# Kernel tuning notes

Measured on AMD Instinct MI355X. Metric: run time of the kernel, lower is better.

## Reference

```python
import jax, jax.numpy as jnp
import numpy as np

V, E, HT, HC = 30000, 300, 256, 256
B, LC, T = 32, 32, 64
NTAG = 9  # output_dim + 2


def lstm_dir(x, lens, Wih, Whh, b, reverse):
    """Variable-length single-direction LSTM (packed-sequence semantics).
    x: [N, T, D], lens: [N] int. Returns outputs [N, T, H] zeroed at pad steps.
    Masked state update keeps h,c frozen at pad steps, so reverse=True starts
    from each sequence's true last element (zeros carry through leading pads).
    """
    N, Tn, _ = x.shape
    H = Whh.shape[1]
    gx = jnp.einsum('ntd,gd->ntg', x, Wih) + b            # [N,T,4H]
    mask = jnp.arange(Tn)[None, :] < lens[:, None]         # [N,T]

    def step(carry, inp):
        h, c = carry
        g_t, m = inp                                       # [N,4H], [N]
        gates = g_t + h @ Whh.T
        i, f, g, o = jnp.split(gates, 4, axis=-1)
        c_new = jax.nn.sigmoid(f) * c + jax.nn.sigmoid(i) * jnp.tanh(g)
        h_new = jax.nn.sigmoid(o) * jnp.tanh(c_new)
        m = m[:, None]
        h2 = jnp.where(m, h_new, h)
        c2 = jnp.where(m, c_new, c)
        return (h2, c2), jnp.where(m, h2, 0.0)

    init = (jnp.zeros((N, H), x.dtype), jnp.zeros((N, H), x.dtype))
    xs = (jnp.swapaxes(gx, 0, 1), mask.T)
    _, ys = jax.lax.scan(step, init, xs, reverse=reverse)
    return jnp.swapaxes(ys, 0, 1)                          # [N,T,H]


def bilstm(x, lens, Wih_f, Whh_f, b_f, Wih_b, Whh_b, b_b):
    hf = lstm_dir(x, lens, Wih_f, Whh_f, b_f, reverse=False)
    hb = lstm_dir(x, lens, Wih_b, Whh_b, b_b, reverse=True)
    return jnp.concatenate([hf, hb], axis=-1)


def setup_inputs() -> dict:
    key = jax.random.key(0)
    ks = jax.random.split(key, 20)
    s = 0.05
    inp = {
        'x': jax.random.randint(ks[0], (B, LC, T), 0, V, dtype=jnp.int32),
        'x_feats': jax.random.normal(ks[1], (B, LC, 64), jnp.float32),
        'x_len': jnp.maximum(jax.random.randint(ks[2], (B,), 0, LC, dtype=jnp.int32), 1),
        'x_chunk_len': jax.random.randint(ks[3], (B, LC), 1, T + 1, dtype=jnp.int32),
        'emb': jax.random.normal(ks[4], (V, E), jnp.float32) * s,
        'tok_Wih_f': jax.random.normal(ks[5], (4 * HT, E), jnp.float32) * s,
        'tok_Whh_f': jax.random.normal(ks[6], (4 * HT, HT), jnp.float32) * s,
        'tok_b_f': jax.random.normal(ks[7], (4 * HT,), jnp.float32) * s,
        'tok_Wih_b': jax.random.normal(ks[8], (4 * HT, E), jnp.float32) * s,
        'tok_Whh_b': jax.random.normal(ks[9], (4 * HT, HT), jnp.float32) * s,
        'tok_b_b': jax.random.normal(ks[10], (4 * HT,), jnp.float32) * s,
        'chk_Wih_f': jax.random.normal(ks[11], (4 * HC, 2 * HT), jnp.float32) * s,
        'chk_Whh_f': jax.random.normal(ks[12], (4 * HC, HC), jnp.float32) * s,
        'chk_b_f': jax.random.normal(ks[13], (4 * HC,), jnp.float32) * s,
        'chk_Wih_b': jax.random.normal(ks[14], (4 * HC, 2 * HT), jnp.float32) * s,
        'chk_Whh_b': jax.random.normal(ks[15], (4 * HC, HC), jnp.float32) * s,
        'chk_b_b': jax.random.normal(ks[16], (4 * HC,), jnp.float32) * s,
        'fc_W': jax.random.normal(ks[17], (NTAG, 2 * HC), jnp.float32) * s,
        'fc_b': jax.random.normal(ks[18], (NTAG,), jnp.float32) * s,
    }
    return inp


def reference(x, x_feats, x_len, x_chunk_len, emb,
              tok_Wih_f, tok_Whh_f, tok_b_f, tok_Wih_b, tok_Whh_b, tok_b_b,
              chk_Wih_f, chk_Whh_f, chk_b_f, chk_Wih_b, chk_Whh_b, chk_b_b,
              fc_W, fc_b):
    b, lc, t = x.shape
    xe = emb[x].reshape(b * lc, t, -1)                     # [B*LC, T, E]
    clens = jnp.clip(x_chunk_len.reshape(-1), 1, t)        # [B*LC]
    h = bilstm(xe, clens, tok_Wih_f, tok_Whh_f, tok_b_f,
               tok_Wih_b, tok_Whh_b, tok_b_b)              # [B*LC, T, 2HT]
    # gather output at last valid timestep (= [fwd final, bwd one-step])
    last = h[jnp.arange(b * lc), clens - 1]                # [B*LC, 2HT]
    chunks = last.reshape(b, lc, -1)                       # [B, LC, 2HT]
    ch = bilstm(chunks, x_len, chk_Wih_f, chk_Whh_f, chk_b_f,
                chk_Wih_b, chk_Whh_b, chk_b_b)             # [B, LC, 2HC]
    # pad_packed(total_length=LC) gives zeros at pad -> fc sees zeros there
    out = ch @ fc_W.T + fc_b                               # [B, LC, NTAG]
    return out
```

## Files before the change

kernel.cpp:

```cpp
#include <hip/hip_runtime.h>


typedef __attribute__((ext_vector_type(8))) short s16x8;
typedef __attribute__((ext_vector_type(4))) float f32x4;
typedef __attribute__((ext_vector_type(2))) unsigned int u32x2;

__device__ __forceinline__ unsigned short f2bf(float f) {
  unsigned u = __builtin_bit_cast(unsigned, f);
  u += 0x7fff + ((u >> 16) & 1);
  return (unsigned short)(u >> 16);
}
__device__ __forceinline__ float bf2f(unsigned short h) {
  unsigned u = ((unsigned)h) << 16;
  return __builtin_bit_cast(float, u);
}
__device__ __forceinline__ float sigm(float x) { return 1.f / (1.f + __expf(-x)); }
__device__ __forceinline__ float tanh_(float x) { return 1.f - 2.f / (__expf(2.f * x) + 1.f); }

union PK8 { s16x8 v; unsigned short u[8]; };

__global__ void prep_weights(const float* __restrict__ wihf, const float* __restrict__ wihb,
                             const float* __restrict__ wcf, const float* __restrict__ wcb,
                             unsigned short* __restrict__ o_wf, unsigned short* __restrict__ o_wb,
                             unsigned short* __restrict__ o_wcf, unsigned short* __restrict__ o_wcb) {
  const int job = blockIdx.y, r = blockIdx.x, tid = threadIdx.x;
  const float* src; unsigned short* dst; int Ks, Kd;
  switch (job) {
    case 0: src = wihf; dst = o_wf;   Ks = 300; Kd = 320; break;
    case 1: src = wihb; dst = o_wb;   Ks = 300; Kd = 320; break;
    case 2: src = wcf;  dst = o_wcf;  Ks = 512; Kd = 512; break;
    default:src = wcb;  dst = o_wcb;  Ks = 512; Kd = 512; break;
  }
  for (int c = tid; c < Kd; c += 256)
    dst[r * Kd + c] = f2bf(c < Ks ? src[r * Ks + c] : 0.f);
}

__global__ __launch_bounds__(256)
void prep_whh_frag(const float* __restrict__ w0, const float* __restrict__ w1,
                   const float* __restrict__ w2,
                   unsigned short* __restrict__ o0, unsigned short* __restrict__ o1,
                   unsigned short* __restrict__ o2) {
  const float* src = blockIdx.y == 0 ? w0 : (blockIdx.y == 1 ? w1 : w2);
  unsigned short* dst = blockIdx.y == 0 ? o0 : (blockIdx.y == 1 ? o1 : o2);
  const int fid = blockIdx.x;
  const int b = fid & 1, g = (fid >> 1) & 3, kt = (fid >> 3) & 7, js = fid >> 6;
  for (int i = threadIdx.x; i < 512; i += 256) {
    const int lane = i >> 3, e = i & 7;
    const int cc = lane & 15, qq = lane >> 4;
    const int row = g * 256 + (js * 2 + b) * 16 + cc;
    const int col = kt * 32 + qq * 8 + e;
    dst[(size_t)fid * 512 + i] = f2bf(src[row * 256 + col]);
  }
}

__global__ void prep_small(const int* __restrict__ x, const int* __restrict__ xcl,
                           int* __restrict__ clens, int* __restrict__ lastv,
                           int* __restrict__ order, int* __restrict__ glen) {
  __shared__ int start[65];
  const int n = threadIdx.x;
  if (n < 65) start[n] = 0;
  __syncthreads();
  int len = xcl[n]; len = len < 1 ? 1 : (len > 64 ? 64 : len);
  clens[n] = len;
  lastv[n] = x[n * 64 + len - 1];
  atomicAdd(&start[len], 1);
  __syncthreads();
  if (n == 0) {
    int acc = 0;
    for (int l = 64; l >= 1; --l) { int h = start[l]; start[l] = acc; acc += h; }
  }
  __syncthreads();
  int pos = atomicAdd(&start[len], 1);
  order[pos] = n;
  __syncthreads();
  if (n < 64) glen[n] = clens[order[n * 16]];
}

__global__ __launch_bounds__(256, 2)
void gemm_bf(const float* __restrict__ A, const int* __restrict__ rowmap,
             int Mrows, int Astride, int Klog, int KP,
             const unsigned short* __restrict__ B, unsigned short* __restrict__ C) {
  __shared__ unsigned short As[128 * 40];
// ... 64 lines not shown
    }
  }
  __syncthreads();
#pragma unroll
  for (int mt = 0; mt < 4; ++mt)
#pragma unroll
    for (int nt = 0; nt < 8; ++nt)
#pragma unroll
      for (int r = 0; r < 4; ++r)
        Ep[w][(mt * 16 + qq * 4 + r) * 136 + nt * 16 + cc] = f2bf(acc[mt][nt][r]);
  __syncthreads();
#pragma unroll
  for (int it = 0; it < 16; ++it) {
    int row = it * 4 + qq;
    s16x8 d = *(const s16x8*)&Ep[w][row * 136 + cc * 8];
    int gm = m0 + wrow * 64 + row;
    int gn = n0 + wcol * 128 + cc * 8;
    if (gm < Mrows) *(s16x8*)&C[(long)gm * 1024 + gn] = d;
  }
}

__global__ void bwd_step(const unsigned short* __restrict__ gxb,
                         const float* __restrict__ bias,
                         float* __restrict__ chunks) {
  const int n = blockIdx.x, j = threadIdx.x;
  const unsigned short* row = gxb + (long)n * 1024;
  float gi = bf2f(row[j]) + bias[j];
  float gg = bf2f(row[512 + j]) + bias[512 + j];
  float go = bf2f(row[768 + j]) + bias[768 + j];
  float cn = sigm(gi) * tanh_(gg);
  chunks[(long)n * 512 + 256 + j] = sigm(go) * tanh_(cn);
}

__global__ __launch_bounds__(256)
void gather_gx(const unsigned short* __restrict__ proj, const int* __restrict__ x,
               const int* __restrict__ order, const int* __restrict__ clens,
               const int* __restrict__ glen, const float* __restrict__ bias,
               unsigned short* __restrict__ gx) {
  const int t = blockIdx.x, p = blockIdx.y, j = threadIdx.x;
  if (t >= glen[p >> 4]) return;
  const int seq = order[p];
  const int len = clens[seq];
  if (t >= len) return;
  unsigned short* dst = gx + (((size_t)(p >> 4) * 64 + t) * 16 + (p & 15)) * 1024 + j * 4;
  const int tok = x[seq * 64 + t];
  const unsigned short* src = proj + (size_t)tok * 1024 + j;
  unsigned v0 = f2bf(bf2f(src[0]) + bias[j]);
  unsigned v1 = f2bf(bf2f(src[256]) + bias[256 + j]);
  unsigned v2 = f2bf(bf2f(src[512]) + bias[512 + j]);
  unsigned v3 = f2bf(bf2f(src[768]) + bias[768 + j]);
  u32x2 pk = {v0 | (v1 << 16), v2 | (v3 << 16)};
  *(u32x2*)dst = pk;
}

__global__ __launch_bounds__(256)
void repack4(const unsigned short* __restrict__ s0, const unsigned short* __restrict__ s1,
             const float* __restrict__ b0, const float* __restrict__ b1,
             unsigned short* __restrict__ d0, unsigned short* __restrict__ d1) {
  const int r = blockIdx.x, j = threadIdx.x;
  const int m = r >> 5, t = r & 31;
  const int mg = m >> 4, m16 = m & 15;
  const unsigned short* s = (blockIdx.y ? s1 : s0) + (size_t)r * 1024;
  const float* bb = blockIdx.y ? b1 : b0;
  unsigned short* d = (blockIdx.y ? d1 : d0) +
                      (size_t)((mg * 32 + t) * 16 + m16) * 1024 + j * 4;
  unsigned v0 = f2bf(bf2f(s[j]) + bb[j]);
  unsigned v1 = f2bf(bf2f(s[256 + j]) + bb[256 + j]);
  unsigned v2 = f2bf(bf2f(s[512 + j]) + bb[512 + j]);
  unsigned v3 = f2bf(bf2f(s[768 + j]) + bb[768 + j]);
  u32x2 pk = {v0 | (v1 << 16), v2 | (v3 << 16)};
  *(u32x2*)d = pk;
}

__global__ __launch_bounds__(1024, 4)
void tok_fwd(const unsigned short* __restrict__ gx,
             const unsigned short* __restrict__ WhP,
             const int* __restrict__ order,
             const int* __restrict__ clens,
             const int* __restrict__ glen,
             float* __restrict__ chunks) {
  extern __shared__ unsigned short smem[];
  unsigned short* hbuf = smem;
  unsigned short* ldsW = smem + 8448;
  int* sg = (int*)(smem + 8448 + 65536);
  int* slen = sg + 16;

  const int tid = threadIdx.x;
  const int lane = tid & 63, w = tid >> 6;
  const int cc = lane & 15, qq = lane >> 4;
  const int gb = blockIdx.x;

  if (tid < 16) {
    int s = order[gb * 16 + tid];
    sg[tid] = s;
    slen[tid] = clens[s];
  }
  for (int i = tid; i < 4224; i += 1024) hbuf[i] = 0;

  const unsigned short* wgl = WhP + ((size_t)(w >> 1) * 64 + (w & 1)) * 512 + lane * 8;
  {
    unsigned short* ld = ldsW + w * 4096 + lane * 8;
#pragma unroll
    for (int kt = 0; kt < 2; ++kt)
#pragma unroll
      for (int g = 0; g < 4; ++g)
        *(s16x8*)&ld[(kt * 4 + g) * 512] = *(const s16x8*)&wgl[(kt * 8 + g * 2) * 512];
  }
  s16x8 Rw[24];
#pragma unroll
  for (int kt = 2; kt < 8; ++kt)
#pragma unroll
    for (int g = 0; g < 4; ++g)
      Rw[(kt - 2) * 4 + g] = *(const s16x8*)&wgl[(kt * 8 + g * 2) * 512];

  __syncthreads();

  const int maxlen = glen[gb];
  const int j = w * 16 + cc;
  int lenr[4];
#pragma unroll
  for (int r = 0; r < 4; ++r) lenr[r] = slen[qq * 4 + r];

  float cst[4];
  unsigned short hreg[4];
#pragma unroll
  for (int r = 0; r < 4; ++r) { cst[r] = 0.f; hreg[r] = 0; }

  const unsigned short* gx0 = gx + (size_t)gb * 64 * 16 * 1024 + j * 4;
  const unsigned short* ldw = ldsW + w * 4096 + lane * 8;
  f32x4 zz = {0.f, 0.f, 0.f, 0.f};

  for (int t = 0; t < maxlen; ++t) {
    const unsigned short* hr = hbuf + (t & 1) * 4224;
    unsigned short* hw = hbuf + ((t & 1) ^ 1) * 4224;

    __syncthreads();

    u32x2 gxp[4];
#pragma unroll
    for (int r = 0; r < 4; ++r)
      gxp[r] = *(const u32x2*)(gx0 + ((size_t)t * 16 + qq * 4 + r) * 1024);

    f32x4 acc[4];
#pragma unroll
    for (int g = 0; g < 4; ++g) acc[g] = zz;

#pragma unroll
    for (int kt = 0; kt < 2; ++kt) {
      s16x8 a0 = *(const s16x8*)&hr[cc * 264 + kt * 32 + qq * 8];
#pragma unroll
      for (int g = 0; g < 4; ++g) {
        s16x8 bf = *(const s16x8*)&ldw[(kt * 4 + g) * 512];
        acc[g] = __builtin_amdgcn_mfma_f32_16x16x32_bf16(a0, bf, acc[g], 0, 0, 0);
      }
    }
#pragma unroll
    for (int kt = 2; kt < 8; ++kt) {
      s16x8 a0 = *(const s16x8*)&hr[cc * 264 + kt * 32 + qq * 8];
#pragma unroll
      for (int g = 0; g < 4; ++g)
        acc[g] = __builtin_amdgcn_mfma_f32_16x16x32_bf16(a0, Rw[(kt - 2) * 4 + g], acc[g], 0, 0, 0);
    }

#pragma unroll
    for (int r = 0; r < 4; ++r) {
      const int m = qq * 4 + r;
      const u32x2 pk = gxp[r];
      float gi = acc[0][r] + bf2f((unsigned short)(pk.x & 0xffff));
      float gf = acc[1][r] + bf2f((unsigned short)(pk.x >> 16));
      float gg = acc[2][r] + bf2f((unsigned short)(pk.y & 0xffff));
      float go = acc[3][r] + bf2f((unsigned short)(pk.y >> 16));
      if (t < lenr[r]) {
        float cn = sigm(gf) * cst[r] + sigm(gi) * tanh_(gg);
        cst[r] = cn;
        hreg[r] = f2bf(sigm(go) * tanh_(cn));
      }
      hw[m * 264 + j] = hreg[r];
    }
  }

#pragma unroll
  for (int r = 0; r < 4; ++r)
    chunks[(size_t)sg[qq * 4 + r] * 512 + j] = bf2f(hreg[r]);
}

__global__ __launch_bounds__(1024, 4)
void chunk_rec(const unsigned short* __restrict__ gxf,
               const unsigned short* __restrict__ gxb,
               const unsigned short* __restrict__ WhPf,
               const unsigned short* __restrict__ WhPb,
               const int* __restrict__ xlen,
               unsigned short* __restrict__ ch) {
  extern __shared__ unsigned short smem[];
  unsigned short* hbuf = smem;
  unsigned short* ldsW = smem + 8448;

  const int tid = threadIdx.x;
  const int lane = tid & 63, w = tid >> 6;
  const int cc = lane & 15, qq = lane >> 4;
  const int dir = blockIdx.x & 1, mg = blockIdx.x >> 1;
  const unsigned short* gx = (dir ? gxb : gxf) + (size_t)mg * 32 * 16 * 1024;
  const unsigned short* WhP = dir ? WhPb : WhPf;

  for (int i = tid; i < 4224; i += 1024) hbuf[i] = 0;

  const unsigned short* wgl = WhP + ((size_t)(w >> 1) * 64 + (w & 1)) * 512 + lane * 8;
  {
    unsigned short* ld = ldsW + w * 4096 + lane * 8;
#pragma unroll
    for (int kt = 0; kt < 2; ++kt)
#pragma unroll
      for (int g = 0; g < 4; ++g)
        *(s16x8*)&ld[(kt * 4 + g) * 512] = *(const s16x8*)&wgl[(kt * 8 + g * 2) * 512];
  }
  s16x8 Rw[24];
#pragma unroll
  for (int kt = 2; kt < 8; ++kt)
#pragma unroll
    for (int g = 0; g < 4; ++g)
      Rw[(kt - 2) * 4 + g] = *(const s16x8*)&wgl[(kt * 8 + g * 2) * 512];

  __syncthreads();

  const int j = w * 16 + cc;
  int lenr[4];
#pragma unroll
  for (int r = 0; r < 4; ++r) {
    int L = xlen[mg * 16 + qq * 4 + r];
    lenr[r] = L > 32 ? 32 : L;
  }

  float cst[4];
  unsigned short hreg[4];
#pragma unroll
  for (int r = 0; r < 4; ++r) { cst[r] = 0.f; hreg[r] = 0; }

  const unsigned short* ldw = ldsW + w * 4096 + lane * 8;
  f32x4 zz = {0.f, 0.f, 0.f, 0.f};

  for (int tt = 0; tt < 32; ++tt) {
    const int t = dir ? (31 - tt) : tt;
    const unsigned short* hr = hbuf + (tt & 1) * 4224;
    unsigned short* hw = hbuf + ((tt & 1) ^ 1) * 4224;

    __syncthreads();

    u32x2 gxp[4];
#pragma unroll
    for (int r = 0; r < 4; ++r)
      gxp[r] = *(const u32x2*)(gx + ((size_t)t * 16 + qq * 4 + r) * 1024 + j * 4);

    f32x4 acc[4];
#pragma unroll
    for (int g = 0; g < 4; ++g) acc[g] = zz;

#pragma unroll
    for (int kt = 0; kt < 2; ++kt) {
      s16x8 a0 = *(const s16x8*)&hr[cc * 264 + kt * 32 + qq * 8];
#pragma unroll
      for (int g = 0; g < 4; ++g) {
        s16x8 bf = *(const s16x8*)&ldw[(kt * 4 + g) * 512];
        acc[g] = __builtin_amdgcn_mfma_f32_16x16x32_bf16(a0, bf, acc[g], 0, 0, 0);
      }
    }
#pragma unroll
    for (int kt = 2; kt < 8; ++kt) {
      s16x8 a0 = *(const s16x8*)&hr[cc * 264 + kt * 32 + qq * 8];
#pragma unroll
      for (int g = 0; g < 4; ++g)
        acc[g] = __builtin_amdgcn_mfma_f32_16x16x32_bf16(a0, Rw[(kt - 2) * 4 + g], acc[g], 0, 0, 0);
    }

#pragma unroll
    for (int r = 0; r < 4; ++r) {
      const int m = qq * 4 + r;
      const u32x2 pk = gxp[r];
      float gi = acc[0][r] + bf2f((unsigned short)(pk.x & 0xffff));
      float gf = acc[1][r] + bf2f((unsigned short)(pk.x >> 16));
      float gg = acc[2][r] + bf2f((unsigned short)(pk.y & 0xffff));
      float go = acc[3][r] + bf2f((unsigned short)(pk.y >> 16));
      unsigned short out16 = 0;
      if (t < lenr[r]) {
        float cn = sigm(gf) * cst[r] + sigm(gi) * tanh_(gg);
        cst[r] = cn;
        hreg[r] = f2bf(sigm(go) * tanh_(cn));
        out16 = hreg[r];
      }
      hw[m * 264 + j] = hreg[r];
      ch[(size_t)((mg * 16 + m) * 32 + t) * 512 + dir * 256 + j] = out16;
    }
  }
}

__global__ __launch_bounds__(64)
void fc_kernel(const unsigned short* __restrict__ ch, const float* __restrict__ W,
               const float* __restrict__ bfc, float* __restrict__ out) {
  const int n = blockIdx.x, lane = threadIdx.x;
  float xv[8];
  const unsigned short* cp = ch + (long)n * 512 + lane * 8;
#pragma unroll
  for (int i = 0; i < 8; ++i) xv[i] = bf2f(cp[i]);
  float s[9];
#pragma unroll
  for (int k = 0; k < 9; ++k) {
    const float* wr = W + k * 512 + lane * 8;
    float t = 0.f;
#pragma unroll
    for (int i = 0; i < 8; ++i) t += xv[i] * wr[i];
    s[k] = t;
  }
#pragma unroll
  for (int off = 32; off; off >>= 1)
#pragma unroll
    for (int k = 0; k < 9; ++k) s[k] += __shfl_down(s[k], off, 64);
  if (lane == 0) {
#pragma unroll
    for (int k = 0; k < 9; ++k) out[n * 9 + k] = s[k] + bfc[k];
  }
}

extern "C" void kernel_launch(void* const* d_in, const int* in_sizes, int n_in,
                              void* d_out, int out_size, void* d_ws, size_t ws_size,
// ... 10 lines not shown
  const float* chk_Wih_f   = (const float*)d_in[11];
  const float* chk_Whh_f   = (const float*)d_in[12];
  const float* chk_b_f     = (const float*)d_in[13];
  const float* chk_Wih_b   = (const float*)d_in[14];
  const float* chk_Whh_b   = (const float*)d_in[15];
  const float* chk_b_b     = (const float*)d_in[16];
  const float* fc_W        = (const float*)d_in[17];
  const float* fc_b        = (const float*)d_in[18];
  float* out = (float*)d_out;

  char* ws = (char*)d_ws;
  size_t off = 0;
  auto alloc = [&](size_t bytes) -> void* {
    void* p = ws + off;
    off += (bytes + 255) & ~(size_t)255;
    return p;
  };
  unsigned short* Wf   = (unsigned short*)alloc((size_t)1024 * 320 * 2);
  unsigned short* Wb   = (unsigned short*)alloc((size_t)1024 * 320 * 2);
  unsigned short* Wcf  = (unsigned short*)alloc((size_t)1024 * 512 * 2);
  unsigned short* Wcb  = (unsigned short*)alloc((size_t)1024 * 512 * 2);
  unsigned short* WhPtok=(unsigned short*)alloc((size_t)512 * 512 * 2);
  unsigned short* WhPcf= (unsigned short*)alloc((size_t)512 * 512 * 2);
  unsigned short* WhPcb= (unsigned short*)alloc((size_t)512 * 512 * 2);
  unsigned short* proj = (unsigned short*)alloc((size_t)30000 * 1024 * 2);
  unsigned short* gxbb = (unsigned short*)alloc((size_t)1024 * 1024 * 2);
  unsigned short* gxcf = (unsigned short*)alloc((size_t)1024 * 1024 * 2);
  unsigned short* gxcb = (unsigned short*)alloc((size_t)1024 * 1024 * 2);
  unsigned short* gxcfp= (unsigned short*)alloc((size_t)1024 * 1024 * 2);
  unsigned short* gxcbp= (unsigned short*)alloc((size_t)1024 * 1024 * 2);
  float*          chunks = (float*)alloc((size_t)1024 * 512 * 4);
  unsigned short* cho  = (unsigned short*)alloc((size_t)1024 * 512 * 2);
  unsigned short* gxs  = (unsigned short*)alloc((size_t)1024 * 64 * 1024 * 2);
  int* clens = (int*)alloc(1024 * 4);
  int* lastv = (int*)alloc(1024 * 4);
  int* order = (int*)alloc(1024 * 4);
  int* glen  = (int*)alloc(64 * 4);

  hipFuncSetAttribute((const void*)tok_fwd,
                      hipFuncAttributeMaxDynamicSharedMemorySize, 148096);
  hipFuncSetAttribute((const void*)chunk_rec,
                      hipFuncAttributeMaxDynamicSharedMemorySize, 147968);

  prep_weights<<<dim3(1024, 4), 256, 0, stream>>>(
      tok_Wih_f, tok_Wih_b, chk_Wih_f, chk_Wih_b, Wf, Wb, Wcf, Wcb);
  prep_whh_frag<<<dim3(512, 3), 256, 0, stream>>>(
      tok_Whh_f, chk_Whh_f, chk_Whh_b, WhPtok, WhPcf, WhPcb);
  prep_small<<<1, 1024, 0, stream>>>(x, x_chunk_len, clens, lastv, order, glen);

  gemm_bf<<<dim3(4, 235), 256, 0, stream>>>(emb, nullptr, 30000, 300, 300, 320, Wf, proj);
  gemm_bf<<<dim3(4, 8), 256, 0, stream>>>(emb, lastv, 1024, 300, 300, 320, Wb, gxbb);
  bwd_step<<<1024, 256, 0, stream>>>(gxbb, tok_b_b, chunks);
  gather_gx<<<dim3(64, 1024), 256, 0, stream>>>(proj, x, order, clens, glen, tok_b_f, gxs);
  tok_fwd<<<64, 1024, 148096, stream>>>(gxs, WhPtok, order, clens, glen, chunks);
  gemm_bf<<<dim3(4, 8), 256, 0, stream>>>(chunks, nullptr, 1024, 512, 512, 512, Wcf, gxcf);
  gemm_bf<<<dim3(4, 8), 256, 0, stream>>>(chunks, nullptr, 1024, 512, 512, 512, Wcb, gxcb);
  repack4<<<dim3(1024, 2), 256, 0, stream>>>(gxcf, gxcb, chk_b_f, chk_b_b, gxcfp, gxcbp);
  chunk_rec<<<4, 1024, 147968, stream>>>(gxcfp, gxcbp, WhPcf, WhPcb, x_len, cho);
  fc_kernel<<<1024, 64, 0, stream>>>(cho, fc_W, fc_b, out);
}
```

Before: 883.6 us.

## Halve recurrent LSTM block size, giving each wave two hidden columns

The token-forward and chunk recurrent kernels drop from 16 waves to 8 waves per block. Each wave now computes 32 hidden units (8 MFMA accumulators) instead of 16, so half as many waves meet at the per-step __syncthreads. The gx layout is permuted in gather_gx/repack4 so each lane can load both columns' gates with one 16-byte read. Weight fragments are split between LDS, 40 registers and 8 global reloads per step. This raises register pressure and adds per-step global weight traffic in exchange for less barrier and wave overhead.

```diff
diff --git a/kernel.cpp b/kernel.cpp
--- a/kernel.cpp
+++ b/kernel.cpp
@@ -4,6 +4,7 @@
 typedef __attribute__((ext_vector_type(8))) short s16x8;
 typedef __attribute__((ext_vector_type(4))) float f32x4;
 typedef __attribute__((ext_vector_type(2))) unsigned int u32x2;
+typedef __attribute__((ext_vector_type(4))) unsigned int u32x4;
 
 __device__ __forceinline__ unsigned short f2bf(float f) {
   unsigned u = __builtin_bit_cast(unsigned, f);
@@ -178,6 +179,10 @@
   chunks[(long)n * 512 + 256 + j] = sigm(go) * tanh_(cn);
 }
 
+__device__ __forceinline__ int gx_perm(int j) {
+  return (j & ~31) + ((j & 15) << 1) + ((j >> 4) & 1);
+}
+
 __global__ __launch_bounds__(256)
 void gather_gx(const unsigned short* __restrict__ proj, const int* __restrict__ x,
                const int* __restrict__ order, const int* __restrict__ clens,
@@ -188,7 +193,7 @@
   const int seq = order[p];
   const int len = clens[seq];
   if (t >= len) return;
-  unsigned short* dst = gx + (((size_t)(p >> 4) * 64 + t) * 16 + (p & 15)) * 1024 + j * 4;
+  unsigned short* dst = gx + (((size_t)(p >> 4) * 64 + t) * 16 + (p & 15)) * 1024 + gx_perm(j) * 4;
   const int tok = x[seq * 64 + t];
   const unsigned short* src = proj + (size_t)tok * 1024 + j;
   unsigned v0 = f2bf(bf2f(src[0]) + bias[j]);
@@ -209,7 +214,7 @@
   const unsigned short* s = (blockIdx.y ? s1 : s0) + (size_t)r * 1024;
   const float* bb = blockIdx.y ? b1 : b0;
   unsigned short* d = (blockIdx.y ? d1 : d0) +
-                      (size_t)((mg * 32 + t) * 16 + m16) * 1024 + j * 4;
+                      (size_t)((mg * 32 + t) * 16 + m16) * 1024 + gx_perm(j) * 4;
   unsigned v0 = f2bf(bf2f(s[j]) + bb[j]);
   unsigned v1 = f2bf(bf2f(s[256 + j]) + bb[256 + j]);
   unsigned v2 = f2bf(bf2f(s[512 + j]) + bb[512 + j]);
@@ -218,7 +223,7 @@
   *(u32x2*)d = pk;
 }
 
-__global__ __launch_bounds__(1024, 4)
+__global__ __launch_bounds__(512, 2)
 void tok_fwd(const unsigned short* __restrict__ gx,
              const unsigned short* __restrict__ WhP,
              const int* __restrict__ order,
@@ -241,39 +246,35 @@
     sg[tid] = s;
     slen[tid] = clens[s];
   }
-  for (int i = tid; i < 4224; i += 1024) hbuf[i] = 0;
-
-  const unsigned short* wgl = WhP + ((size_t)(w >> 1) * 64 + (w & 1)) * 512 + lane * 8;
+  for (int i = tid; i < 4224; i += 512) hbuf[i] = 0;
+
+  const unsigned short* wgl = WhP + (size_t)w * 64 * 512 + lane * 8;
   {
-    unsigned short* ld = ldsW + w * 4096 + lane * 8;
-#pragma unroll
-    for (int kt = 0; kt < 2; ++kt)
-#pragma unroll
-      for (int g = 0; g < 4; ++g)
-        *(s16x8*)&ld[(kt * 4 + g) * 512] = *(const s16x8*)&wgl[(kt * 8 + g * 2) * 512];
-  }
-  s16x8 Rw[24];
-#pragma unroll
-  for (int kt = 2; kt < 8; ++kt)
-#pragma unroll
-    for (int g = 0; g < 4; ++g)
-      Rw[(kt - 2) * 4 + g] = *(const s16x8*)&wgl[(kt * 8 + g * 2) * 512];
+    unsigned short* ld = ldsW + w * 8192 + lane * 8;
+#pragma unroll
+    for (int s = 0; s < 16; ++s)
+      *(s16x8*)&ld[s * 512] = *(const s16x8*)&wgl[s * 512];
+  }
+  s16x8 Rw[40];
+#pragma unroll
+  for (int s = 0; s < 40; ++s)
+    Rw[s] = *(const s16x8*)&wgl[(16 + s) * 512];
 
   __syncthreads();
 
   const int maxlen = glen[gb];
-  const int j = w * 16 + cc;
   int lenr[4];
 #pragma unroll
   for (int r = 0; r < 4; ++r) lenr[r] = slen[qq * 4 + r];
 
-  float cst[4];
-  unsigned short hreg[4];
-#pragma unroll
-  for (int r = 0; r < 4; ++r) { cst[r] = 0.f; hreg[r] = 0; }
-
-  const unsigned short* gx0 = gx + (size_t)gb * 64 * 16 * 1024 + j * 4;
-  const unsigned short* ldw = ldsW + w * 4096 + lane * 8;
+  float cst[8];
+  unsigned short hreg[8];
+#pragma unroll
+  for (int i = 0; i < 8; ++i) { cst[i] = 0.f; hreg[i] = 0; }
+
+  const int j0 = w * 32 + cc;
+  const unsigned short* gx0 = gx + (size_t)gb * 64 * 16 * 1024 + (w * 32 + cc * 2) * 4;
+  const unsigned short* ldw = ldsW + w * 8192 + lane * 8;
   f32x4 zz = {0.f, 0.f, 0.f, 0.f};
 
   for (int t = 0; t < maxlen; ++t) {
@@ -282,55 +283,81 @@
 
     __syncthreads();
 
-    u32x2 gxp[4];
+    s16x8 W7[4];
+#pragma unroll
+    for (int s = 0; s < 4; ++s)
+      W7[s] = *(const s16x8*)&wgl[(56 + s) * 512];
+
+    u32x4 gxp[4];
 #pragma unroll
     for (int r = 0; r < 4; ++r)
-      gxp[r] = *(const u32x2*)(gx0 + ((size_t)t * 16 + qq * 4 + r) * 1024);
-
-    f32x4 acc[4];
-#pragma unroll
-    for (int g = 0; g < 4; ++g) acc[g] = zz;
+      gxp[r] = *(const u32x4*)(gx0 + ((size_t)t * 16 + qq * 4 + r) * 1024);
+
+    f32x4 acc[8];
+#pragma unroll
+    for (int s = 0; s < 8; ++s) acc[s] = zz;
 
 #pragma unroll
     for (int kt = 0; kt < 2; ++kt) {
       s16x8 a0 = *(const s16x8*)&hr[cc * 264 + kt * 32 + qq * 8];
 #pragma unroll
-      for (int g = 0; g < 4; ++g) {
-        s16x8 bf = *(const s16x8*)&ldw[(kt * 4 + g) * 512];
-        acc[g] = __builtin_amdgcn_mfma_f32_16x16x32_bf16(a0, bf, acc[g], 0, 0, 0);
-      }
-    }
-#pragma unroll
-    for (int kt = 2; kt < 8; ++kt) {
+      for (int s = 0; s < 8; ++s)
+        acc[s] = __builtin_amdgcn_mfma_f32_16x16x32_bf16(
+            a0, *(const s16x8*)&ldw[(kt * 8 + s) * 512], acc[s], 0, 0, 0);
+    }
+#pragma unroll
+    for (int kt = 2; kt < 7; ++kt) {
       s16x8 a0 = *(const s16x8*)&hr[cc * 264 + kt * 32 + qq * 8];
 #pragma unroll
-      for (int g = 0; g < 4; ++g)
-        acc[g] = __builtin_amdgcn_mfma_f32_16x16x32_bf16(a0, Rw[(kt - 2) * 4 + g], acc[g], 0, 0, 0);
+      for (int s = 0; s < 8; ++s)
+        acc[s] = __builtin_amdgcn_mfma_f32_16x16x32_bf16(
+            a0, Rw[(kt - 2) * 8 + s], acc[s], 0, 0, 0);
+    }
+    {
+      s16x8 a7 = *(const s16x8*)&hr[cc * 264 + 7 * 32 + qq * 8];
+#pragma unroll
+      for (int s = 0; s < 4; ++s)
+        acc[s] = __builtin_amdgcn_mfma_f32_16x16x32_bf16(a7, W7[s], acc[s], 0, 0, 0);
+#pragma unroll
+      for (int s = 0; s < 4; ++s)
+        W7[s] = *(const s16x8*)&wgl[(60 + s) * 512];
+#pragma unroll
+      for (int s = 0; s < 4; ++s)
+        acc[4 + s] = __builtin_amdgcn_mfma_f32_16x16x32_bf16(a7, W7[s], acc[4 + s], 0, 0, 0);
     }
 
 #pragma unroll
     for (int r = 0; r < 4; ++r) {
       const int m = qq * 4 + r;
-      const u32x2 pk = gxp[r];
-      float gi = acc[0][r] + bf2f((unsigned short)(pk.x & 0xffff));
-      float gf = acc[1][r] + bf2f((unsigned short)(pk.x >> 16));
-      float gg = acc[2][r] + bf2f((unsigned short)(pk.y & 0xffff));
-      float go = acc[3][r] + bf2f((unsigned short)(pk.y >> 16));
-      if (t < lenr[r]) {
-        float cn = sigm(gf) * cst[r] + sigm(gi) * tanh_(gg);
-        cst[r] = cn;
-        hreg[r] = f2bf(sigm(go) * tanh_(cn));
+      const bool upd = t < lenr[r];
+      const u32x4 pk = gxp[r];
+#pragma unroll
+      for (int jj = 0; jj < 2; ++jj) {
+        const unsigned lo = jj ? pk.z : pk.x;
+        const unsigned hi = jj ? pk.w : pk.y;
+        float gi = acc[0 * 2 + jj][r] + bf2f((unsigned short)(lo & 0xffff));
+        float gf = acc[1 * 2 + jj][r] + bf2f((unsigned short)(lo >> 16));
+        float gg = acc[2 * 2 + jj][r] + bf2f((unsigned short)(hi & 0xffff));
+        float go = acc[3 * 2 + jj][r] + bf2f((unsigned short)(hi >> 16));
+        const int si = r * 2 + jj;
+        if (upd) {
+          float cn = sigm(gf) * cst[si] + sigm(gi) * tanh_(gg);
+          cst[si] = cn;
+          hreg[si] = f2bf(sigm(go) * tanh_(cn));
+        }
+        hw[m * 264 + j0 + jj * 16] = hreg[si];
       }
-      hw[m * 264 + j] = hreg[r];
     }
   }
 
 #pragma unroll
   for (int r = 0; r < 4; ++r)
-    chunks[(size_t)sg[qq * 4 + r] * 512 + j] = bf2f(hreg[r]);
-}
-
-__global__ __launch_bounds__(1024, 4)
+#pragma unroll
+    for (int jj = 0; jj < 2; ++jj)
+      chunks[(size_t)sg[qq * 4 + r] * 512 + j0 + jj * 16] = bf2f(hreg[r * 2 + jj]);
+}
+
+__global__ __launch_bounds__(512, 2)
 void chunk_rec(const unsigned short* __restrict__ gxf,
                const unsigned short* __restrict__ gxb,
                const unsigned short* __restrict__ WhPf,
@@ -345,30 +372,27 @@
   const int lane = tid & 63, w = tid >> 6;
   const int cc = lane & 15, qq = lane >> 4;
   const int dir = blockIdx.x & 1, mg = blockIdx.x >> 1;
-  const unsigned short* gx = (dir ? gxb : gxf) + (size_t)mg * 32 * 16 * 1024;
+  const unsigned short* gx = (dir ? gxb : gxf) + (size_t)mg * 32 * 16 * 1024
+                             + (w * 32 + cc * 2) * 4;
   const unsigned short* WhP = dir ? WhPb : WhPf;
 
-  for (int i = tid; i < 4224; i += 1024) hbuf[i] = 0;
-
-  const unsigned short* wgl = WhP + ((size_t)(w >> 1) * 64 + (w & 1)) * 512 + lane * 8;
+  for (int i = tid; i < 4224; i += 512) hbuf[i] = 0;
+
+  const unsigned short* wgl = WhP + (size_t)w * 64 * 512 + lane * 8;
   {
-    unsigned short* ld = ldsW + w * 4096 + lane * 8;
-#pragma unroll
-    for (int kt = 0; kt < 2; ++kt)
-#pragma unroll
-      for (int g = 0; g < 4; ++g)
-        *(s16x8*)&ld[(kt * 4 + g) * 512] = *(const s16x8*)&wgl[(kt * 8 + g * 2) * 512];
-  }
-  s16x8 Rw[24];
-#pragma unroll
-  for (int kt = 2; kt < 8; ++kt)
-#pragma unroll
-    for (int g = 0; g < 4; ++g)
-      Rw[(kt - 2) * 4 + g] = *(const s16x8*)&wgl[(kt * 8 + g * 2) * 512];
-
-  __syncthreads();
-
-  const int j = w * 16 + cc;
+    unsigned short* ld = ldsW + w * 8192 + lane * 8;
+#pragma unroll
+    for (int s = 0; s < 16; ++s)
+      *(s16x8*)&ld[s * 512] = *(const s16x8*)&wgl[s * 512];
+  }
+  s16x8 Rw[40];
+#pragma unroll
+  for (int s = 0; s < 40; ++s)
+    Rw[s] = *(const s16x8*)&wgl[(16 + s) * 512];
+
+  __syncthreads();
+
+  const int j0 = w * 32 + cc;
   int lenr[4];
 #pragma unroll
   for (int r = 0; r < 4; ++r) {
@@ -376,12 +400,12 @@
     lenr[r] = L > 32 ? 32 : L;
   }
 
-  float cst[4];
-  unsigned short hreg[4];
-#pragma unroll
-  for (int r = 0; r < 4; ++r) { cst[r] = 0.f; hreg[r] = 0; }
-
-  const unsigned short* ldw = ldsW + w * 4096 + lane * 8;
+  float cst[8];
+  unsigned short hreg[8];
+#pragma unroll
+  for (int i = 0; i < 8; ++i) { cst[i] = 0.f; hreg[i] = 0; }
+
+  const unsigned short* ldw = ldsW + w * 8192 + lane * 8;
   f32x4 zz = {0.f, 0.f, 0.f, 0.f};
 
   for (int tt = 0; tt < 32; ++tt) {
@@ -391,49 +415,73 @@
 
     __syncthreads();
 
-    u32x2 gxp[4];
+    s16x8 W7[4];
+#pragma unroll
+    for (int s = 0; s < 4; ++s)
+      W7[s] = *(const s16x8*)&wgl[(56 + s) * 512];
+
+    u32x4 gxp[4];
 #pragma unroll
     for (int r = 0; r < 4; ++r)
-      gxp[r] = *(const u32x2*)(gx + ((size_t)t * 16 + qq * 4 + r) * 1024 + j * 4);
-
-    f32x4 acc[4];
-#pragma unroll
-    for (int g = 0; g < 4; ++g) acc[g] = zz;
+      gxp[r] = *(const u32x4*)(gx + ((size_t)t * 16 + qq * 4 + r) * 1024);
+
+    f32x4 acc[8];
+#pragma unroll
+    for (int s = 0; s < 8; ++s) acc[s] = zz;
 
 #pragma unroll
     for (int kt = 0; kt < 2; ++kt) {
       s16x8 a0 = *(const s16x8*)&hr[cc * 264 + kt * 32 + qq * 8];
 #pragma unroll
-      for (int g = 0; g < 4; ++g) {
-        s16x8 bf = *(const s16x8*)&ldw[(kt * 4 + g) * 512];
-        acc[g] = __builtin_amdgcn_mfma_f32_16x16x32_bf16(a0, bf, acc[g], 0, 0, 0);
-      }
-    }
-#pragma unroll
-    for (int kt = 2; kt < 8; ++kt) {
+      for (int s = 0; s < 8; ++s)
+        acc[s] = __builtin_amdgcn_mfma_f32_16x16x32_bf16(
+            a0, *(const s16x8*)&ldw[(kt * 8 + s) * 512], acc[s], 0, 0, 0);
+    }
+#pragma unroll
+    for (int kt = 2; kt < 7; ++kt) {
       s16x8 a0 = *(const s16x8*)&hr[cc * 264 + kt * 32 + qq * 8];
 #pragma unroll
-      for (int g = 0; g < 4; ++g)
-        acc[g] = __builtin_amdgcn_mfma_f32_16x16x32_bf16(a0, Rw[(kt - 2) * 4 + g], acc[g], 0, 0, 0);
+      for (int s = 0; s < 8; ++s)
+        acc[s] = __builtin_amdgcn_mfma_f32_16x16x32_bf16(
+            a0, Rw[(kt - 2) * 8 + s], acc[s], 0, 0, 0);
+    }
+    {
+      s16x8 a7 = *(const s16x8*)&hr[cc * 264 + 7 * 32 + qq * 8];
+#pragma unroll
+      for (int s = 0; s < 4; ++s)
+        acc[s] = __builtin_amdgcn_mfma_f32_16x16x32_bf16(a7, W7[s], acc[s], 0, 0, 0);
+#pragma unroll
+      for (int s = 0; s < 4; ++s)
+        W7[s] = *(const s16x8*)&wgl[(60 + s) * 512];
+#pragma unroll
+      for (int s = 0; s < 4; ++s)
+        acc[4 + s] = __builtin_amdgcn_mfma_f32_16x16x32_bf16(a7, W7[s], acc[4 + s], 0, 0, 0);
     }
 
 #pragma unroll
     for (int r = 0; r < 4; ++r) {
       const int m = qq * 4 + r;
-      const u32x2 pk = gxp[r];
-      float gi = acc[0][r] + bf2f((unsigned short)(pk.x & 0xffff));
-      float gf = acc[1][r] + bf2f((unsigned short)(pk.x >> 16));
-      float gg = acc[2][r] + bf2f((unsigned short)(pk.y & 0xffff));
-      float go = acc[3][r] + bf2f((unsigned short)(pk.y >> 16));
-      unsigned short out16 = 0;
-      if (t < lenr[r]) {
-        float cn = sigm(gf) * cst[r] + sigm(gi) * tanh_(gg);
-        cst[r] = cn;
-        hreg[r] = f2bf(sigm(go) * tanh_(cn));
-        out16 = hreg[r];
+      const bool upd = t < lenr[r];
+      const u32x4 pk = gxp[r];
+#pragma unroll
+      for (int jj = 0; jj < 2; ++jj) {
+        const unsigned lo = jj ? pk.z : pk.x;
+        const unsigned hi = jj ? pk.w : pk.y;
+        float gi = acc[0 * 2 + jj][r] + bf2f((unsigned short)(lo & 0xffff));
+        float gf = acc[1 * 2 + jj][r] + bf2f((unsigned short)(lo >> 16));
+        float gg = acc[2 * 2 + jj][r] + bf2f((unsigned short)(hi & 0xffff));
+        float go = acc[3 * 2 + jj][r] + bf2f((unsigned short)(hi >> 16));
+        const int si = r * 2 + jj;
+        unsigned short out16 = 0;
+        if (upd) {
+          float cn = sigm(gf) * cst[si] + sigm(gi) * tanh_(gg);
+          cst[si] = cn;
+          hreg[si] = f2bf(sigm(go) * tanh_(cn));
+          out16 = hreg[si];
+        }
+        hw[m * 264 + j0 + jj * 16] = hreg[si];
+        ch[(size_t)((mg * 16 + m) * 32 + t) * 512 + dir * 256 + j0 + jj * 16] = out16;
       }
-      hw[m * 264 + j] = hreg[r];
-      ch[(size_t)((mg * 16 + m) * 32 + t) * 512 + dir * 256 + j] = out16;
     }
   }
 }
@@ -530,10 +578,10 @@
   gemm_bf<<<dim3(4, 8), 256, 0, stream>>>(emb, lastv, 1024, 300, 300, 320, Wb, gxbb);
   bwd_step<<<1024, 256, 0, stream>>>(gxbb, tok_b_b, chunks);
   gather_gx<<<dim3(64, 1024), 256, 0, stream>>>(proj, x, order, clens, glen, tok_b_f, gxs);
-  tok_fwd<<<64, 1024, 148096, stream>>>(gxs, WhPtok, order, clens, glen, chunks);
+  tok_fwd<<<64, 512, 148096, stream>>>(gxs, WhPtok, order, clens, glen, chunks);
   gemm_bf<<<dim3(4, 8), 256, 0, stream>>>(chunks, nullptr, 1024, 512, 512, 512, Wcf, gxcf);
   gemm_bf<<<dim3(4, 8), 256, 0, stream>>>(chunks, nullptr, 1024, 512, 512, 512, Wcb, gxcb);
   repack4<<<dim3(1024, 2), 256, 0, stream>>>(gxcf, gxcb, chk_b_f, chk_b_b, gxcfp, gxcbp);
-  chunk_rec<<<4, 1024, 147968, stream>>>(gxcfp, gxcbp, WhPcf, WhPcb, x_len, cho);
+  chunk_rec<<<4, 512, 147968, stream>>>(gxcfp, gxcbp, WhPcf, WhPcb, x_len, cho);
   fc_kernel<<<1024, 64, 0, stream>>>(cho, fc_W, fc_b, out);
 }
```

New measurement: 798.4 us. 1.11x faster.

## Split each LSTM recurrence across two cooperating blocks exchanging hidden halves via global flags

Applied to the files above, without the earlier changes.

Each recurrent group is now handled by two 512-thread blocks instead of one 1024-thread block. Each block computes half of the hidden units and keeps its own half of Whh in LDS. It fetches the partner's half of h through a global scratch buffer, synchronised with release/acquire step counters. The partner's weights are streamed from global memory each step instead of being held in registers. The goal is to double the number of active CUs and cut per-step work, at the cost of cross-block spin-waits that depend on both partner blocks being co-resident.

```diff
diff --git a/kernel.cpp b/kernel.cpp
--- a/kernel.cpp
+++ b/kernel.cpp
@@ -4,6 +4,7 @@
 typedef __attribute__((ext_vector_type(8))) short s16x8;
 typedef __attribute__((ext_vector_type(4))) float f32x4;
 typedef __attribute__((ext_vector_type(2))) unsigned int u32x2;
+typedef __attribute__((ext_vector_type(4))) unsigned int u32x4;
 
 __device__ __forceinline__ unsigned short f2bf(float f) {
   unsigned u = __builtin_bit_cast(unsigned, f);
@@ -43,11 +44,11 @@
   const float* src = blockIdx.y == 0 ? w0 : (blockIdx.y == 1 ? w1 : w2);
   unsigned short* dst = blockIdx.y == 0 ? o0 : (blockIdx.y == 1 ? o1 : o2);
   const int fid = blockIdx.x;
-  const int b = fid & 1, g = (fid >> 1) & 3, kt = (fid >> 3) & 7, js = fid >> 6;
+  const int g = fid & 3, kt = (fid >> 2) & 7, jt = fid >> 5;
   for (int i = threadIdx.x; i < 512; i += 256) {
     const int lane = i >> 3, e = i & 7;
     const int cc = lane & 15, qq = lane >> 4;
-    const int row = g * 256 + (js * 2 + b) * 16 + cc;
+    const int row = g * 256 + jt * 16 + cc;
     const int col = kt * 32 + qq * 8 + e;
     dst[(size_t)fid * 512 + i] = f2bf(src[row * 256 + col]);
   }
@@ -218,51 +219,47 @@
   *(u32x2*)d = pk;
 }
 
-__global__ __launch_bounds__(1024, 4)
+__global__ __launch_bounds__(512)
 void tok_fwd(const unsigned short* __restrict__ gx,
              const unsigned short* __restrict__ WhP,
              const int* __restrict__ order,
              const int* __restrict__ clens,
              const int* __restrict__ glen,
+             unsigned short* __restrict__ xh,
+             unsigned int* __restrict__ cnt,
              float* __restrict__ chunks) {
   extern __shared__ unsigned short smem[];
   unsigned short* hbuf = smem;
-  unsigned short* ldsW = smem + 8448;
-  int* sg = (int*)(smem + 8448 + 65536);
+  unsigned short* ldsW = smem + 4352;
+  int* sg = (int*)(smem + 4352 + 65536);
   int* slen = sg + 16;
 
   const int tid = threadIdx.x;
   const int lane = tid & 63, w = tid >> 6;
   const int cc = lane & 15, qq = lane >> 4;
-  const int gb = blockIdx.x;
+  const int b = blockIdx.x;
+  const int g = (b & 7) | ((b >> 4) << 3);
+  const int half = (b >> 3) & 1;
 
   if (tid < 16) {
-    int s = order[gb * 16 + tid];
+    int s = order[g * 16 + tid];
     sg[tid] = s;
     slen[tid] = clens[s];
   }
-  for (int i = tid; i < 4224; i += 1024) hbuf[i] = 0;
-
-  const unsigned short* wgl = WhP + ((size_t)(w >> 1) * 64 + (w & 1)) * 512 + lane * 8;
+  for (int i = tid; i < 4352; i += 512) hbuf[i] = 0;
+
+  const int jt = half * 8 + w;
+  const unsigned short* wOwn = WhP + ((size_t)(jt * 8 + half * 4) * 4) * 512 + lane * 8;
+  const unsigned short* wPar = WhP + ((size_t)(jt * 8 + (1 - half) * 4) * 4) * 512 + lane * 8;
   {
-    unsigned short* ld = ldsW + w * 4096 + lane * 8;
-#pragma unroll
-    for (int kt = 0; kt < 2; ++kt)
-#pragma unroll
-      for (int g = 0; g < 4; ++g)
-        *(s16x8*)&ld[(kt * 4 + g) * 512] = *(const s16x8*)&wgl[(kt * 8 + g * 2) * 512];
-  }
-  s16x8 Rw[24];
-#pragma unroll
-  for (int kt = 2; kt < 8; ++kt)
-#pragma unroll
-    for (int g = 0; g < 4; ++g)
-      Rw[(kt - 2) * 4 + g] = *(const s16x8*)&wgl[(kt * 8 + g * 2) * 512];
-
-  __syncthreads();
-
-  const int maxlen = glen[gb];
-  const int j = w * 16 + cc;
+    unsigned short* ld = ldsW + w * 8192 + lane * 8;
+#pragma unroll
+    for (int s = 0; s < 16; ++s)
+      *(s16x8*)&ld[s * 512] = *(const s16x8*)&wOwn[s * 512];
+  }
+  __syncthreads();
+
+  const int maxlen = glen[g];
   int lenr[4];
 #pragma unroll
   for (int r = 0; r < 4; ++r) lenr[r] = slen[qq * 4 + r];
@@ -270,44 +267,78 @@
   float cst[4];
   unsigned short hreg[4];
 #pragma unroll
-  for (int r = 0; r < 4; ++r) { cst[r] = 0.f; hreg[r] = 0; }
-
-  const unsigned short* gx0 = gx + (size_t)gb * 64 * 16 * 1024 + j * 4;
-  const unsigned short* ldw = ldsW + w * 4096 + lane * 8;
+  for (int i = 0; i < 4; ++i) { cst[i] = 0.f; hreg[i] = 0; }
+
+  const int jl = w * 16 + cc;
+  const unsigned short* gx0 = gx + (size_t)g * 64 * 16 * 1024 + (half * 128 + jl) * 4;
+  const unsigned short* ldw = ldsW + w * 8192 + lane * 8;
+  unsigned int* cme = cnt + b;
+  unsigned int* cpp = cnt + (b ^ 8);
+  unsigned short* xh_me = xh + (size_t)(g * 2 + half) * 2 * 2048;
+  const unsigned short* xh_p = xh + (size_t)(g * 2 + (1 - half)) * 2 * 2048;
   f32x4 zz = {0.f, 0.f, 0.f, 0.f};
 
   for (int t = 0; t < maxlen; ++t) {
-    const unsigned short* hr = hbuf + (t & 1) * 4224;
-    unsigned short* hw = hbuf + ((t & 1) ^ 1) * 4224;
+    const unsigned short* hr = hbuf + (t & 1) * 2176;
+    unsigned short* hw = hbuf + ((t & 1) ^ 1) * 2176;
 
     __syncthreads();
-
+    if (t && tid == 0)
+      __hip_atomic_store(cme, (unsigned)t, __ATOMIC_RELEASE, __HIP_MEMORY_SCOPE_AGENT);
+
+    s16x8 S[4], T[4];
+    if (t) {
+#pragma unroll
+      for (int i2 = 0; i2 < 4; ++i2) S[i2] = *(const s16x8*)&wPar[i2 * 512];
+    }
     u32x2 gxp[4];
 #pragma unroll
     for (int r = 0; r < 4; ++r)
       gxp[r] = *(const u32x2*)(gx0 + ((size_t)t * 16 + qq * 4 + r) * 1024);
+    if (t) {
+#pragma unroll
+      for (int i2 = 0; i2 < 4; ++i2) T[i2] = *(const s16x8*)&wPar[(4 + i2) * 512];
+    }
 
     f32x4 acc[4];
 #pragma unroll
-    for (int g = 0; g < 4; ++g) acc[g] = zz;
-
-#pragma unroll
-    for (int kt = 0; kt < 2; ++kt) {
-      s16x8 a0 = *(const s16x8*)&hr[cc * 264 + kt * 32 + qq * 8];
-#pragma unroll
-      for (int g = 0; g < 4; ++g) {
-        s16x8 bf = *(const s16x8*)&ldw[(kt * 4 + g) * 512];
-        acc[g] = __builtin_amdgcn_mfma_f32_16x16x32_bf16(a0, bf, acc[g], 0, 0, 0);
-      }
-    }
-#pragma unroll
-    for (int kt = 2; kt < 8; ++kt) {
-      s16x8 a0 = *(const s16x8*)&hr[cc * 264 + kt * 32 + qq * 8];
-#pragma unroll
-      for (int g = 0; g < 4; ++g)
-        acc[g] = __builtin_amdgcn_mfma_f32_16x16x32_bf16(a0, Rw[(kt - 2) * 4 + g], acc[g], 0, 0, 0);
-    }
-
+    for (int i2 = 0; i2 < 4; ++i2) acc[i2] = zz;
+
+#pragma unroll
+    for (int s = 0; s < 4; ++s) {
+      s16x8 a = *(const s16x8*)&hr[cc * 136 + s * 32 + qq * 8];
+#pragma unroll
+      for (int g4 = 0; g4 < 4; ++g4)
+        acc[g4] = __builtin_amdgcn_mfma_f32_16x16x32_bf16(
+            a, *(const s16x8*)&ldw[(s * 4 + g4) * 512], acc[g4], 0, 0, 0);
+    }
+
+    if (t) {
+      while (__hip_atomic_load(cpp, __ATOMIC_ACQUIRE, __HIP_MEMORY_SCOPE_AGENT) < (unsigned)t) {}
+      const unsigned short* xp = xh_p + ((t + 1) & 1) * 2048;
+      s16x8 a0 = *(const s16x8*)(xp + cc * 128 + 0 * 32 + qq * 8);
+      s16x8 a1 = *(const s16x8*)(xp + cc * 128 + 1 * 32 + qq * 8);
+      s16x8 a2 = *(const s16x8*)(xp + cc * 128 + 2 * 32 + qq * 8);
+      s16x8 a3 = *(const s16x8*)(xp + cc * 128 + 3 * 32 + qq * 8);
+#pragma unroll
+      for (int g4 = 0; g4 < 4; ++g4)
+        acc[g4] = __builtin_amdgcn_mfma_f32_16x16x32_bf16(a0, S[g4], acc[g4], 0, 0, 0);
+#pragma unroll
+      for (int i2 = 0; i2 < 4; ++i2) S[i2] = *(const s16x8*)&wPar[(8 + i2) * 512];
+#pragma unroll
+      for (int g4 = 0; g4 < 4; ++g4)
+        acc[g4] = __builtin_amdgcn_mfma_f32_16x16x32_bf16(a1, T[g4], acc[g4], 0, 0, 0);
+#pragma unroll
+      for (int i2 = 0; i2 < 4; ++i2) T[i2] = *(const s16x8*)&wPar[(12 + i2) * 512];
+#pragma unroll
+      for (int g4 = 0; g4 < 4; ++g4)
+        acc[g4] = __builtin_amdgcn_mfma_f32_16x16x32_bf16(a2, S[g4], acc[g4], 0, 0, 0);
+#pragma unroll
+      for (int g4 = 0; g4 < 4; ++g4)
+        acc[g4] = __builtin_amdgcn_mfma_f32_16x16x32_bf16(a3, T[g4], acc[g4], 0, 0, 0);
+    }
+
+    unsigned short* xme = xh_me + (t & 1) * 2048;
 #pragma unroll
     for (int r = 0; r < 4; ++r) {
       const int m = qq * 4 + r;
@@ -321,54 +352,50 @@
         cst[r] = cn;
         hreg[r] = f2bf(sigm(go) * tanh_(cn));
       }
-      hw[m * 264 + j] = hreg[r];
+      hw[m * 136 + jl] = hreg[r];
+      xme[m * 128 + jl] = hreg[r];
     }
   }
 
 #pragma unroll
   for (int r = 0; r < 4; ++r)
-    chunks[(size_t)sg[qq * 4 + r] * 512 + j] = bf2f(hreg[r]);
-}
-
-__global__ __launch_bounds__(1024, 4)
+    chunks[(size_t)sg[qq * 4 + r] * 512 + half * 128 + jl] = bf2f(hreg[r]);
+}
+
+__global__ __launch_bounds__(512)
 void chunk_rec(const unsigned short* __restrict__ gxf,
                const unsigned short* __restrict__ gxb,
                const unsigned short* __restrict__ WhPf,
                const unsigned short* __restrict__ WhPb,
                const int* __restrict__ xlen,
+               unsigned short* __restrict__ xh,
+               unsigned int* __restrict__ cnt,
                unsigned short* __restrict__ ch) {
   extern __shared__ unsigned short smem[];
   unsigned short* hbuf = smem;
-  unsigned short* ldsW = smem + 8448;
+  unsigned short* ldsW = smem + 4352;
 
   const int tid = threadIdx.x;
   const int lane = tid & 63, w = tid >> 6;
   const int cc = lane & 15, qq = lane >> 4;
-  const int dir = blockIdx.x & 1, mg = blockIdx.x >> 1;
+  const int b = blockIdx.x;
+  const int dir = b & 1, mg = (b >> 1) & 1, half = (b >> 2) & 1;
   const unsigned short* gx = (dir ? gxb : gxf) + (size_t)mg * 32 * 16 * 1024;
   const unsigned short* WhP = dir ? WhPb : WhPf;
 
-  for (int i = tid; i < 4224; i += 1024) hbuf[i] = 0;
-
-  const unsigned short* wgl = WhP + ((size_t)(w >> 1) * 64 + (w & 1)) * 512 + lane * 8;
+  for (int i = tid; i < 4352; i += 512) hbuf[i] = 0;
+
+  const int jt = half * 8 + w;
+  const unsigned short* wOwn = WhP + ((size_t)(jt * 8 + half * 4) * 4) * 512 + lane * 8;
+  const unsigned short* wPar = WhP + ((size_t)(jt * 8 + (1 - half) * 4) * 4) * 512 + lane * 8;
   {
-    unsigned short* ld = ldsW + w * 4096 + lane * 8;
-#pragma unroll
-    for (int kt = 0; kt < 2; ++kt)
-#pragma unroll
-      for (int g = 0; g < 4; ++g)
-        *(s16x8*)&ld[(kt * 4 + g) * 512] = *(const s16x8*)&wgl[(kt * 8 + g * 2) * 512];
-  }
-  s16x8 Rw[24];
-#pragma unroll
-  for (int kt = 2; kt < 8; ++kt)
-#pragma unroll
-    for (int g = 0; g < 4; ++g)
-      Rw[(kt - 2) * 4 + g] = *(const s16x8*)&wgl[(kt * 8 + g * 2) * 512];
-
-  __syncthreads();
-
-  const int j = w * 16 + cc;
+    unsigned short* ld = ldsW + w * 8192 + lane * 8;
+#pragma unroll
+    for (int s = 0; s < 16; ++s)
+      *(s16x8*)&ld[s * 512] = *(const s16x8*)&wOwn[s * 512];
+  }
+  __syncthreads();
+
   int lenr[4];
 #pragma unroll
   for (int r = 0; r < 4; ++r) {
@@ -379,44 +406,79 @@
   float cst[4];
   unsigned short hreg[4];
 #pragma unroll
-  for (int r = 0; r < 4; ++r) { cst[r] = 0.f; hreg[r] = 0; }
-
-  const unsigned short* ldw = ldsW + w * 4096 + lane * 8;
+  for (int i = 0; i < 4; ++i) { cst[i] = 0.f; hreg[i] = 0; }
+
+  const int jl = w * 16 + cc;
+  const unsigned short* gxl = gx + (half * 128 + jl) * 4;
+  const unsigned short* ldw = ldsW + w * 8192 + lane * 8;
+  unsigned int* cme = cnt + b;
+  unsigned int* cpp = cnt + (b ^ 4);
+  unsigned short* xh_me = xh + (size_t)((b & 3) * 2 + half) * 2 * 2048;
+  const unsigned short* xh_p = xh + (size_t)((b & 3) * 2 + (1 - half)) * 2 * 2048;
   f32x4 zz = {0.f, 0.f, 0.f, 0.f};
 
   for (int tt = 0; tt < 32; ++tt) {
     const int t = dir ? (31 - tt) : tt;
-    const unsigned short* hr = hbuf + (tt & 1) * 4224;
-    unsigned short* hw = hbuf + ((tt & 1) ^ 1) * 4224;
+    const unsigned short* hr = hbuf + (tt & 1) * 2176;
+    unsigned short* hw = hbuf + ((tt & 1) ^ 1) * 2176;
 
     __syncthreads();
-
+    if (tt && tid == 0)
+      __hip_atomic_store(cme, (unsigned)tt, __ATOMIC_RELEASE, __HIP_MEMORY_SCOPE_AGENT);
+
+    s16x8 S[4], T[4];
+    if (tt) {
+#pragma unroll
+      for (int i2 = 0; i2 < 4; ++i2) S[i2] = *(const s16x8*)&wPar[i2 * 512];
+    }
     u32x2 gxp[4];
 #pragma unroll
     for (int r = 0; r < 4; ++r)
-      gxp[r] = *(const u32x2*)(gx + ((size_t)t * 16 + qq * 4 + r) * 1024 + j * 4);
+      gxp[r] = *(const u32x2*)(gxl + ((size_t)t * 16 + qq * 4 + r) * 1024);
+    if (tt) {
+#pragma unroll
+      for (int i2 = 0; i2 < 4; ++i2) T[i2] = *(const s16x8*)&wPar[(4 + i2) * 512];
+    }
 
     f32x4 acc[4];
 #pragma unroll
-    for (int g = 0; g < 4; ++g) acc[g] = zz;
-
-#pragma unroll
-    for (int kt = 0; kt < 2; ++kt) {
-      s16x8 a0 = *(const s16x8*)&hr[cc * 264 + kt * 32 + qq * 8];
-#pragma unroll
-      for (int g = 0; g < 4; ++g) {
-        s16x8 bf = *(const s16x8*)&ldw[(kt * 4 + g) * 512];
-        acc[g] = __builtin_amdgcn_mfma_f32_16x16x32_bf16(a0, bf, acc[g], 0, 0, 0);
-      }
-    }
-#pragma unroll
-    for (int kt = 2; kt < 8; ++kt) {
-      s16x8 a0 = *(const s16x8*)&hr[cc * 264 + kt * 32 + qq * 8];
-#pragma unroll
-      for (int g = 0; g < 4; ++g)
-        acc[g] = __builtin_amdgcn_mfma_f32_16x16x32_bf16(a0, Rw[(kt - 2) * 4 + g], acc[g], 0, 0, 0);
-    }
-
+    for (int i2 = 0; i2 < 4; ++i2) acc[i2] = zz;
+
+#pragma unroll
+    for (int s = 0; s < 4; ++s) {
+      s16x8 a = *(const s16x8*)&hr[cc * 136 + s * 32 + qq * 8];
+#pragma unroll
+      for (int g4 = 0; g4 < 4; ++g4)
+        acc[g4] = __builtin_amdgcn_mfma_f32_16x16x32_bf16(
+            a, *(const s16x8*)&ldw[(s * 4 + g4) * 512], acc[g4], 0, 0, 0);
+    }
+
+    if (tt) {
+      while (__hip_atomic_load(cpp, __ATOMIC_ACQUIRE, __HIP_MEMORY_SCOPE_AGENT) < (unsigned)tt) {}
+      const unsigned short* xp = xh_p + ((tt + 1) & 1) * 2048;
+      s16x8 a0 = *(const s16x8*)(xp + cc * 128 + 0 * 32 + qq * 8);
+      s16x8 a1 = *(const s16x8*)(xp + cc * 128 + 1 * 32 + qq * 8);
+      s16x8 a2 = *(const s16x8*)(xp + cc * 128 + 2 * 32 + qq * 8);
+      s16x8 a3 = *(const s16x8*)(xp + cc * 128 + 3 * 32 + qq * 8);
+#pragma unroll
+      for (int g4 = 0; g4 < 4; ++g4)
+        acc[g4] = __builtin_amdgcn_mfma_f32_16x16x32_bf16(a0, S[g4], acc[g4], 0, 0, 0);
+#pragma unroll
+      for (int i2 = 0; i2 < 4; ++i2) S[i2] = *(const s16x8*)&wPar[(8 + i2) * 512];
+#pragma unroll
+      for (int g4 = 0; g4 < 4; ++g4)
+        acc[g4] = __builtin_amdgcn_mfma_f32_16x16x32_bf16(a1, T[g4], acc[g4], 0, 0, 0);
+#pragma unroll
+      for (int i2 = 0; i2 < 4; ++i2) T[i2] = *(const s16x8*)&wPar[(12 + i2) * 512];
+#pragma unroll
+      for (int g4 = 0; g4 < 4; ++g4)
+        acc[g4] = __builtin_amdgcn_mfma_f32_16x16x32_bf16(a2, S[g4], acc[g4], 0, 0, 0);
+#pragma unroll
+      for (int g4 = 0; g4 < 4; ++g4)
+        acc[g4] = __builtin_amdgcn_mfma_f32_16x16x32_bf16(a3, T[g4], acc[g4], 0, 0, 0);
+    }
+
+    unsigned short* xme = xh_me + (tt & 1) * 2048;
 #pragma unroll
     for (int r = 0; r < 4; ++r) {
       const int m = qq * 4 + r;
@@ -432,8 +494,9 @@
         hreg[r] = f2bf(sigm(go) * tanh_(cn));
         out16 = hreg[r];
       }
-      hw[m * 264 + j] = hreg[r];
-      ch[(size_t)((mg * 16 + m) * 32 + t) * 512 + dir * 256 + j] = out16;
+      hw[m * 136 + jl] = hreg[r];
+      xme[m * 128 + jl] = hreg[r];
+      ch[(size_t)((mg * 16 + m) * 32 + t) * 512 + dir * 256 + half * 128 + jl] = out16;
     }
   }
 }
@@ -510,15 +573,22 @@
   float*          chunks = (float*)alloc((size_t)1024 * 512 * 4);
   unsigned short* cho  = (unsigned short*)alloc((size_t)1024 * 512 * 2);
   unsigned short* gxs  = (unsigned short*)alloc((size_t)1024 * 64 * 1024 * 2);
+  unsigned short* xhT  = (unsigned short*)alloc((size_t)64 * 2 * 2 * 2048 * 2);
+  unsigned short* xhC  = (unsigned short*)alloc((size_t)8 * 2 * 2048 * 2);
+  unsigned int* cntT = (unsigned int*)alloc(128 * 4);
+  unsigned int* cntC = (unsigned int*)alloc(8 * 4);
   int* clens = (int*)alloc(1024 * 4);
   int* lastv = (int*)alloc(1024 * 4);
   int* order = (int*)alloc(1024 * 4);
   int* glen  = (int*)alloc(64 * 4);
 
   hipFuncSetAttribute((const void*)tok_fwd,
-                      hipFuncAttributeMaxDynamicSharedMemorySize, 148096);
+                      hipFuncAttributeMaxDynamicSharedMemorySize, 139904);
   hipFuncSetAttribute((const void*)chunk_rec,
-                      hipFuncAttributeMaxDynamicSharedMemorySize, 147968);
+                      hipFuncAttributeMaxDynamicSharedMemorySize, 139776);
+
+  hipMemsetAsync(cntT, 0, 128 * 4, stream);
+  hipMemsetAsync(cntC, 0, 8 * 4, stream);
 
   prep_weights<<<dim3(1024, 4), 256, 0, stream>>>(
       tok_Wih_f, tok_Wih_b, chk_Wih_f, chk_Wih_b, Wf, Wb, Wcf, Wcb);
@@ -530,10 +600,10 @@
   gemm_bf<<<dim3(4, 8), 256, 0, stream>>>(emb, lastv, 1024, 300, 300, 320, Wb, gxbb);
   bwd_step<<<1024, 256, 0, stream>>>(gxbb, tok_b_b, chunks);
   gather_gx<<<dim3(64, 1024), 256, 0, stream>>>(proj, x, order, clens, glen, tok_b_f, gxs);
-  tok_fwd<<<64, 1024, 148096, stream>>>(gxs, WhPtok, order, clens, glen, chunks);
+  tok_fwd<<<128, 512, 139904, stream>>>(gxs, WhPtok, order, clens, glen, xhT, cntT, chunks);
   gemm_bf<<<dim3(4, 8), 256, 0, stream>>>(chunks, nullptr, 1024, 512, 512, 512, Wcf, gxcf);
   gemm_bf<<<dim3(4, 8), 256, 0, stream>>>(chunks, nullptr, 1024, 512, 512, 512, Wcb, gxcb);
   repack4<<<dim3(1024, 2), 256, 0, stream>>>(gxcf, gxcb, chk_b_f, chk_b_b, gxcfp, gxcbp);
-  chunk_rec<<<4, 1024, 147968, stream>>>(gxcfp, gxcbp, WhPcf, WhPcb, x_len, cho);
+  chunk_rec<<<8, 512, 139776, stream>>>(gxcfp, gxcbp, WhPcf, WhPcb, x_len, xhC, cntC, cho);
   fc_kernel<<<1024, 64, 0, stream>>>(cho, fc_W, fc_b, out);
 }
```

Result: slower. 991.5 us (+12.2%).
